# Optimization experiments

Hardware: AMD Instinct MI355X
Metric: run time of the kernel (lower is better)

The kernel has to match this reference:

```python
import jax, jax.numpy as jnp
import numpy as np

B, QL, KVL = 2, 1024, 2048
D = 4096          # hidden_size
NH, NKV = 32, 8   # attention heads / kv heads
HD = D // NH      # head_dim = 128
INNER = 4 * D     # SwiGLU intermediate = 16384
EPS = 1e-5
THETA = 10000.0


def rope_cos_sin(seq_len, head_dim, theta):
    inv_freq = 1.0 / (theta ** (jnp.arange(0, head_dim, 2, dtype=jnp.float32) / head_dim))
    t = jnp.arange(seq_len, dtype=jnp.float32)
    freqs = jnp.outer(t, inv_freq)                      # [S, HD/2]
    emb = jnp.concatenate([freqs, freqs], axis=-1)      # [S, HD]
    return jnp.cos(emb), jnp.sin(emb)


def rotate_half(x):
    half = x.shape[-1] // 2
    return jnp.concatenate([-x[..., half:], x[..., :half]], axis=-1)


def apply_rope(x, cos, sin):
    # x: [B, H, S, HD]; cos/sin: [S, HD] broadcast over batch & heads
    return x * cos[None, None] + rotate_half(x) * sin[None, None]


def layernorm(x, w, b):
    mu = jnp.mean(x, axis=-1, keepdims=True)
    var = jnp.var(x, axis=-1, keepdims=True)
    return (x - mu) * jax.lax.rsqrt(var + EPS) * w + b


def setup_inputs() -> dict:
    key = jax.random.key(0)
    ks = jax.random.split(key, 12)
    s = 0.02
    return {
        "hidden_states": jax.random.normal(ks[0], (B, QL, D), jnp.float32),
        "encoder_hidden_states": jax.random.normal(ks[1], (B, KVL, D), jnp.float32),
        "encoder_attention_mask": jnp.ones((B, KVL), jnp.float32),
        "ln1_w": jnp.ones((D,), jnp.float32),
        "ln1_b": jnp.zeros((D,), jnp.float32),
        "q_w": jax.random.normal(ks[2], (D, D), jnp.float32) * s,        # [out, in]
        "k_w": jax.random.normal(ks[3], (NKV * HD, D), jnp.float32) * s,
        "v_w": jax.random.normal(ks[4], (NKV * HD, D), jnp.float32) * s,
        "o_w": jax.random.normal(ks[5], (D, D), jnp.float32) * s,
        "ln2_w": jnp.ones((D,), jnp.float32),
        "ln2_b": jnp.zeros((D,), jnp.float32),
        "gate_w": jax.random.normal(ks[6], (INNER, D), jnp.float32) * s,
        "up_w": jax.random.normal(ks[7], (INNER, D), jnp.float32) * s,
        "down_w": jax.random.normal(ks[8], (D, INNER), jnp.float32) * s,
    }


def reference(hidden_states, encoder_hidden_states, encoder_attention_mask,
              ln1_w, ln1_b, q_w, k_w, v_w, o_w, ln2_w, ln2_b,
              gate_w, up_w, down_w):
    residual = hidden_states
    h = layernorm(hidden_states, ln1_w, ln1_b)

    # projections
    q = (h @ q_w.T).reshape(B, QL, NH, HD).transpose(0, 2, 1, 3)                    # [B,NH,QL,HD]
    k = (encoder_hidden_states @ k_w.T).reshape(B, KVL, NKV, HD).transpose(0, 2, 1, 3)  # [B,NKV,KVL,HD]
    v = (encoder_hidden_states @ v_w.T).reshape(B, KVL, NKV, HD).transpose(0, 2, 1, 3)

    # RoPE: q uses positions 0..QL-1, k uses positions 0..KVL-1 (position_ids=None -> cos[None])
    q_cos, q_sin = rope_cos_sin(QL, HD, THETA)
    kv_cos, kv_sin = rope_cos_sin(KVL, HD, THETA)
    q = apply_rope(q, q_cos, q_sin)
    k = apply_rope(k, kv_cos, kv_sin)

    # GQA repeat_kv: each kv head repeated num_key_value_groups times consecutively
    n_rep = NH // NKV
    k = jnp.repeat(k, n_rep, axis=1)  # [B,NH,KVL,HD]
    v = jnp.repeat(v, n_rep, axis=1)

    attn = jnp.einsum('bhqd,bhkd->bhqk', q, k) / np.sqrt(HD).astype(np.float32)
    # NOTE: original code ADDS the boolean mask (True -> +1.0) to the logits
    mask = (encoder_attention_mask != 0).astype(attn.dtype)  # [B,KVL]
    attn = attn + mask[:, None, None, :]
    attn = jax.nn.softmax(attn.astype(jnp.float32), axis=-1).astype(q.dtype)

    out = jnp.einsum('bhqk,bhkd->bhqd', attn, v)        # [B,NH,QL,HD]
    out = out.transpose(0, 2, 1, 3).reshape(B, QL, D)
    attn_out = out @ o_w.T

    h = residual + attn_out
    residual = h
    h = layernorm(h, ln2_w, ln2_b)
    ff = (jax.nn.silu(h @ gate_w.T) * (h @ up_w.T)) @ down_w.T
    return residual + ff
```

## Files before the change

### kernel.cpp

```cpp
#include <hip/hip_runtime.h>
#include <hip/hip_bf16.h>
#include <math.h>

using bf16 = __hip_bfloat16;
typedef __bf16 bfv8 __attribute__((ext_vector_type(8)));
typedef float f32x4 __attribute__((ext_vector_type(4)));

__device__ __forceinline__ f32x4 mfma16(bfv8 a, bfv8 b, f32x4 c) {
    return __builtin_amdgcn_mfma_f32_16x16x32_bf16(a, b, c, 0, 0, 0);
}

__device__ __forceinline__ void gload_lds16(const void* g, void* l) {
    __builtin_amdgcn_global_load_lds(
        (const __attribute__((address_space(1))) void*)g,
        (__attribute__((address_space(3))) void*)l, 16, 0, 0);
}

__global__ void cvt_kernel(const float* __restrict__ in, bf16* __restrict__ out, long n8) {
    long u = (long)blockIdx.x * 256 + threadIdx.x;
    if (u >= n8) return;
    const float4* p = (const float4*)in + u * 2;
    float4 a = p[0], b = p[1];
    bf16 t8[8] = { __float2bfloat16(a.x), __float2bfloat16(a.y), __float2bfloat16(a.z), __float2bfloat16(a.w),
                   __float2bfloat16(b.x), __float2bfloat16(b.y), __float2bfloat16(b.z), __float2bfloat16(b.w) };
    *(int4*)(out + u * 8) = *(const int4*)t8;
}

__global__ void cvt2_kernel(const float* __restrict__ in1, bf16* __restrict__ out1,
                            const float* __restrict__ in2, bf16* __restrict__ out2, long n8) {
    long u = (long)blockIdx.x * 256 + threadIdx.x;
    const float* in = in1;
    bf16* out = out1;
    if (u >= n8) { u -= n8; in = in2; out = out2; }
    const float4* p = (const float4*)in + u * 2;
    float4 a = p[0], b = p[1];
    bf16 t8[8] = { __float2bfloat16(a.x), __float2bfloat16(a.y), __float2bfloat16(a.z), __float2bfloat16(a.w),
                   __float2bfloat16(b.x), __float2bfloat16(b.y), __float2bfloat16(b.z), __float2bfloat16(b.w) };
    *(int4*)(out + u * 8) = *(const int4*)t8;
}

__global__ void layernorm_kernel(const float* __restrict__ x, const float* __restrict__ gw,
                                 const float* __restrict__ gb, bf16* __restrict__ out)
{
    const int D = 4096;
    int row = blockIdx.x, t = threadIdx.x;
    const float4* xr = (const float4*)(x + (size_t)row * D);
    float4 v[4];
    float s1 = 0.f, s2 = 0.f;
#pragma unroll
    for (int j = 0; j < 4; ++j) {
        v[j] = xr[t + j * 256];
        s1 += v[j].x + v[j].y + v[j].z + v[j].w;
        s2 += v[j].x * v[j].x + v[j].y * v[j].y + v[j].z * v[j].z + v[j].w * v[j].w;
    }
#pragma unroll
    for (int d = 1; d < 64; d <<= 1) { s1 += __shfl_xor(s1, d); s2 += __shfl_xor(s2, d); }
    __shared__ float red[8];
    int wave = t >> 6, lane = t & 63;
    if (lane == 0) { red[wave] = s1; red[4 + wave] = s2; }
    __syncthreads();
    s1 = red[0] + red[1] + red[2] + red[3];
    s2 = red[4] + red[5] + red[6] + red[7];
    float mu = s1 * (1.f / 4096.f);
    float var = s2 * (1.f / 4096.f) - mu * mu;
    float rs = rsqrtf(var + 1e-5f);
    bf16* orow = out + (size_t)row * D;
#pragma unroll
    for (int j = 0; j < 4; ++j) {
        int base = (t + j * 256) * 4;
        float xs[4] = { v[j].x, v[j].y, v[j].z, v[j].w };
        bf16 o4[4];
#pragma unroll
        for (int c = 0; c < 4; ++c)
            o4[c] = __float2bfloat16((xs[c] - mu) * rs * gw[base + c] + gb[base + c]);
        *(int2*)(orow + base) = *(const int2*)o4;
    }
}

__global__ void rope_kernel(bf16* __restrict__ x, int nheads, int seqlen, long total) {
    long idx = (long)blockIdx.x * 256 + threadIdx.x;
    if (idx >= total) return;
    int j = (int)(idx & 63);
    long t2 = idx >> 6;
    int h = (int)(t2 % nheads);
    long row = t2 / nheads;
    int pos = (int)(row % seqlen);
    float inv = exp2f(-(float)j * 0.20762050593046015f);
    float ang = (float)pos * inv;
    float s, c;
    sincosf(ang, &s, &c);
    bf16* p = x + row * ((long)nheads * 128) + (long)h * 128 + j;
    float x0 = __bfloat162float(p[0]);
    float x1 = __bfloat162float(p[64]);
    p[0]  = __float2bfloat16(x0 * c - x1 * s);
    p[64] = __float2bfloat16(x1 * c + x0 * s);
}

template<int BM, int BN, int MODE, bool DUAL, int CM, int CN, int XN>
__global__ __launch_bounds__(512, 2) void gemm_p(
        const bf16* __restrict__ A, const bf16* __restrict__ W, const bf16* __restrict__ W2,
        void* __restrict__ Cout, void* __restrict__ Cout2, const void* __restrict__ aux,
        int M, int N, int K, int Nsplit,
        int ngemm, const float* __restrict__ cf1, bf16* __restrict__ cd1, long cn1,
        const float* __restrict__ cf2, bf16* __restrict__ cd2, long cn2)
{
    const int t = threadIdx.x;
    if ((int)blockIdx.x >= ngemm) {
        const long nb = (long)gridDim.x - ngemm;
        const long tot = cn1 + cn2;
        for (long u = (long)((int)blockIdx.x - ngemm) * 512 + t; u < tot; u += nb * 512) {
            const float* in = cf1;
            bf16* op = cd1;
            long v = u;
            if (v >= cn1) { v -= cn1; in = cf2; op = cd2; }
            float4 a = ((const float4*)in)[v * 2];
            float4 b = ((const float4*)in)[v * 2 + 1];
            bf16 t8[8] = { __float2bfloat16(a.x), __float2bfloat16(a.y),
                           __float2bfloat16(a.z), __float2bfloat16(a.w),
                           __float2bfloat16(b.x), __float2bfloat16(b.y),
                           __float2bfloat16(b.z), __float2bfloat16(b.w) };
            *(int4*)(op + v * 8) = *(const int4*)t8;
        }
        return;
    }

    constexpr int MF = BM / 32;
    constexpr int NF = BN / 64;
    constexpr int ALD = BM / 128;
    constexpr int BLD = BN / 128;
    constexpr int SLD = ALD + BLD;
    __shared__ bf16 lds[3][(BM + BN) * 32];

    const int wid = t >> 6, lane = t & 63;
    const int lr = lane & 15, lg = lane >> 4;
    const int wr = wid >> 2, wc = wid & 3;
    const int bid = blockIdx.x;
    const int xcd = bid & 7, slot = bid >> 3;
    const int sm = slot / CN, sn = slot % CN;
    const int xm = xcd / XN, xn = xcd % XN;
    const int bm = (xm * CM + sm) * BM;
    const int bn = (xn * CN + sn) * BN;

    auto stage = [&](int tt, int buf) {
        const int k0 = tt * 32;
        char* ldsA = (char*)&lds[buf][0];
#pragma unroll
        for (int c = 0; c < ALD; ++c) {
            int Wb = (t + c * 512) * 16;
            int L = Wb ^ (((Wb >> 7) & 7) << 4);
            int row = L >> 6, colb = L & 63;
            gload_lds16(A + (size_t)(bm + row) * K + k0 + (colb >> 1), ldsA + Wb);
        }
        char* ldsB = (char*)&lds[buf][BM * 32];
#pragma unroll
        for (int c = 0; c < BLD; ++c) {
            int Wb = (t + c * 512) * 16;
            int L = Wb ^ (((Wb >> 7) & 7) << 4);
            int row = L >> 6, colb = L & 63;
            const bf16* src;
            if constexpr (DUAL) {
                int nr = bn + row;
                src = (nr >= Nsplit) ? W2 + (size_t)(nr - Nsplit) * K + k0 + (colb >> 1)
                                     : W  + (size_t)nr * K + k0 + (colb >> 1);
            } else {
                src = W + (size_t)(bn + row) * K + k0 + (colb >> 1);
            }
            gload_lds16(src, ldsB + Wb);
        }
    };

    const f32x4 zero4 = { 0.f, 0.f, 0.f, 0.f };
    f32x4 acc[MF][NF];
#pragma unroll
    for (int m = 0; m < MF; ++m)
#pragma unroll
        for (int n = 0; n < NF; ++n) acc[m][n] = zero4;

    const int T = K >> 5;
    stage(0, 0);
    stage(1, 1);
    if constexpr (SLD == 4) asm volatile("s_waitcnt vmcnt(4)" ::: "memory");
    else                    asm volatile("s_waitcnt vmcnt(3)" ::: "memory");
    __builtin_amdgcn_s_barrier();
    __builtin_amdgcn_sched_barrier(0);

    for (int tt = 0; tt < T; ++tt) {
        const int buf = tt % 3;
        bfv8 af[MF], bfr[NF];
#pragma unroll
        for (int m = 0; m < MF; ++m) {
            int row = wr * (BM / 2) + m * 16 + lr;
            int U = row * 64 + lg * 16;
            af[m] = *(const bfv8*)((const char*)&lds[buf][0] + (U ^ (((U >> 7) & 7) << 4)));
        }
#pragma unroll
        for (int n = 0; n < NF; ++n) {
            int row = wc * (BN / 4) + n * 16 + lr;
            int U = row * 64 + lg * 16;
            bfr[n] = *(const bfv8*)((const char*)&lds[buf][BM * 32] + (U ^ (((U >> 7) & 7) << 4)));
        }
        if (tt + 2 < T) stage(tt + 2, (tt + 2) % 3);
        __builtin_amdgcn_s_setprio(1);
#pragma unroll
        for (int m = 0; m < MF; ++m)
#pragma unroll
            for (int n = 0; n < NF; ++n)
                acc[m][n] = mfma16(af[m], bfr[n], acc[m][n]);
        __builtin_amdgcn_s_setprio(0);
        if (tt + 2 < T) {
            if constexpr (SLD == 4) asm volatile("s_waitcnt vmcnt(4)" ::: "memory");
            else                    asm volatile("s_waitcnt vmcnt(3)" ::: "memory");
        } else {
            asm volatile("s_waitcnt vmcnt(0)" ::: "memory");
        }
        __builtin_amdgcn_s_barrier();
        __builtin_amdgcn_sched_barrier(0);
    }

    const int r0 = bm + wr * (BM / 2), c0 = bn + wc * (BN / 4);
#pragma unroll
    for (int m = 0; m < MF; ++m)
#pragma unroll
        for (int n = 0; n < NF; ++n)
#pragma unroll
            for (int i = 0; i < 4; ++i) {
                int r = r0 + m * 16 + lg * 4 + i;
                int c = c0 + n * 16 + lr;
                float a = acc[m][n][i];
                if constexpr (DUAL) {
                    if (c < Nsplit) ((bf16*)Cout)[(size_t)r * Nsplit + c] = __float2bfloat16(a);
                    else ((bf16*)Cout2)[(size_t)r * (N - Nsplit) + (c - Nsplit)] = __float2bfloat16(a);
                } else {
                    size_t idx = (size_t)r * N + c;
                    if constexpr (MODE == 0) {
                        ((bf16*)Cout)[idx] = __float2bfloat16(a);
                    } else if constexpr (MODE == 1) {
                        a = a / (1.f + expf(-a));
                        ((bf16*)Cout)[idx] = __float2bfloat16(a);
                    } else if constexpr (MODE == 2) {
                        a *= __bfloat162float(((const bf16*)aux)[idx]);
                        ((bf16*)Cout)[idx] = __float2bfloat16(a);
                    } else {
                        ((float*)Cout)[idx] = a + ((const float*)aux)[idx];
                    }
                }
            }
}

template<int BN, int MODE, bool DUAL, int CM, int CN, int XN>
__global__ __launch_bounds__(512, 1) void gemm8(
        const bf16* __restrict__ A, const bf16* __restrict__ W, const bf16* __restrict__ W2,
        void* __restrict__ Cout, void* __restrict__ Cout2, const void* __restrict__ aux,
        int M, int N, int K, int Nsplit)
{
    constexpr bool BIG = (BN == 256);
    constexpr int NBUF = BIG ? 2 : 3;
    constexpr int ABY = 32768;
    constexpr int BBY = BN * 128;
    constexpr int TBY = ABY + BBY;
    __shared__ alignas(16) char lds8[NBUF * TBY];

    const int t = threadIdx.x;
    const int wid = t >> 6, lane = t & 63;
    const int lr = lane & 15, lg = lane >> 4;
    const int wrB = wid >> 2, wcB = wid & 3;
    const int wr4 = wid >> 1, wc4 = wid & 1;
    const int bid = blockIdx.x;
    const int xcd = bid & 7, slot = bid >> 3;
    const int sm = slot / CN, sn = slot % CN;
    const int xm = xcd / XN, xn = xcd % XN;
    const int bm = (xm * CM + sm) * 256;
    const int bn = (xn * CN + sn) * BN;

    auto stA = [&](int kt, int h, int buf) {
#pragma unroll
        for (int c = 0; c < 2; ++c) {
            int Wb = (t + c * 512) * 16;
            int L = Wb ^ (((Wb >> 7) & 7) << 4);
            gload_lds16(A + (size_t)(bm + h * 128 + (L >> 7)) * K + kt * 64 + ((L & 127) >> 1),
                        lds8 + buf * TBY + h * 16384 + Wb);
        }
    };
    auto stB = [&](int kt, int h, int buf) {
#pragma unroll
        for (int c = 0; c < 2; ++c) {
            int Wb = (t + c * 512) * 16;
            int L = Wb ^ (((Wb >> 7) & 7) << 4);
            int nr = bn + h * 128 + (L >> 7);
            const bf16* src;
            if constexpr (DUAL) {
                src = (nr >= Nsplit) ? W2 + (size_t)(nr - Nsplit) * K + kt * 64 + ((L & 127) >> 1)
                                     : W  + (size_t)nr * K + kt * 64 + ((L & 127) >> 1);
            } else {
                src = W + (size_t)nr * K + kt * 64 + ((L & 127) >> 1);
            }
            gload_lds16(src, lds8 + buf * TBY + ABY + h * 16384 + Wb);
        }
    };

    const f32x4 zero4 = { 0.f, 0.f, 0.f, 0.f };
    f32x4 acc[BIG ? 8 : 4][4];
#pragma unroll
    for (int m = 0; m < (BIG ? 8 : 4); ++m)
#pragma unroll
        for (int n = 0; n < 4; ++n) acc[m][n] = zero4;

    bfv8 af[4][2], bfr[2][2][2];
    bfv8 afs[2][2], bfs[4][2];

#define LOADA(BUF, MH) do {                                                   \
    const char* _ba = lds8 + (BUF) * TBY;                                     \
    _Pragma("unroll") for (int m = 0; m < 4; ++m)                             \
    _Pragma("unroll") for (int ks = 0; ks < 2; ++ks) {                        \
        int row = wrB * 128 + (MH) * 64 + m * 16 + lr;                        \
        int U = row * 128 + ks * 64 + lg * 16;                                \
        af[m][ks] = *(const bfv8*)(_ba + (U ^ ((row & 7) << 4)));             \
    } } while (0)

#define LOADB(BUF, NH) do {                                                   \
    const char* _bb = lds8 + (BUF) * TBY + ABY;                               \
    _Pragma("unroll") for (int n = 0; n < 2; ++n)                             \
    _Pragma("unroll") for (int ks = 0; ks < 2; ++ks) {                        \
        int row = wcB * 64 + (NH) * 32 + n * 16 + lr;                         \
        int U = row * 128 + ks * 64 + lg * 16;                                \
        bfr[NH][n][ks] = *(const bfv8*)(_bb + (U ^ ((row & 7) << 4)));        \
    } } while (0)

#define MFMAQ(MH, NH) do {                                                    \
    _Pragma("unroll") for (int m = 0; m < 4; ++m)                             \
    _Pragma("unroll") for (int n = 0; n < 2; ++n) {                           \
        acc[(MH)*4+m][(NH)*2+n] = mfma16(af[m][0], bfr[NH][n][0], acc[(MH)*4+m][(NH)*2+n]); \
        acc[(MH)*4+m][(NH)*2+n] = mfma16(af[m][1], bfr[NH][n][1], acc[(MH)*4+m][(NH)*2+n]); \
    } } while (0)

#define LOADA_S(BUF, MH) do {                                                 \
    const char* _ba = lds8 + (BUF) * TBY;                                     \
    _Pragma("unroll") for (int m = 0; m < 2; ++m)                             \
    _Pragma("unroll") for (int ks = 0; ks < 2; ++ks) {                        \
        int row = wr4 * 64 + (MH) * 32 + m * 16 + lr;                         \
        int U = row * 128 + ks * 64 + lg * 16;                                \
        afs[m][ks] = *(const bfv8*)(_ba + (U ^ ((row & 7) << 4)));            \
    } } while (0)

#define LOADB_S(BUF) do {                                                     \
    const char* _bb = lds8 + (BUF) * TBY + ABY;                               \
    _Pragma("unroll") for (int n = 0; n < 4; ++n)                             \
    _Pragma("unroll") for (int ks = 0; ks < 2; ++ks) {                        \
        int row = wc4 * 64 + n * 16 + lr;                                     \
        int U = row * 128 + ks * 64 + lg * 16;                                \
        bfs[n][ks] = *(const bfv8*)(_bb + (U ^ ((row & 7) << 4)));            \
    } } while (0)

#define MFMAQ_S(MH) do {                                                      \
    _Pragma("unroll") for (int m = 0; m < 2; ++m)                             \
    _Pragma("unroll") for (int n = 0; n < 4; ++n) {                           \
        acc[(MH)*2+m][n] = mfma16(afs[m][0], bfs[n][0], acc[(MH)*2+m][n]);    \
        acc[(MH)*2+m][n] = mfma16(afs[m][1], bfs[n][1], acc[(MH)*2+m][n]);    \
    } } while (0)

#define PH_TOP() do { __builtin_amdgcn_s_barrier();                           \
    asm volatile("s_waitcnt lgkmcnt(0)" ::: "memory");                        \
    __builtin_amdgcn_sched_barrier(0);                                        \
    __builtin_amdgcn_s_setprio(1); } while (0)

#define PH_END() do { __builtin_amdgcn_s_setprio(0);                          \
    __builtin_amdgcn_s_barrier(); } while (0)

#define GATE(LIVE) do { __builtin_amdgcn_s_setprio(0);                        \
    if (LIVE) { if constexpr (BIG) asm volatile("s_waitcnt vmcnt(4)" ::: "memory"); \
                else               asm volatile("s_waitcnt vmcnt(6)" ::: "memory"); } \
    else      asm volatile("s_waitcnt vmcnt(0)" ::: "memory");                \
    __builtin_amdgcn_s_barrier(); } while (0)

    const int T = K >> 6;
    const int T2 = T >> 1;

    if constexpr (BIG) {
        stA(0, 0, 0); stA(0, 1, 0); stB(0, 0, 0); stB(0, 1, 0);
        stB(1, 0, 1); stB(1, 1, 1);
        asm volatile("s_waitcnt vmcnt(4)" ::: "memory");
        __builtin_amdgcn_s_barrier();

        for (int tt = 0; tt < T2; ++tt) {
            const int o = 2 * tt + 1, e2 = 2 * tt + 2, o2 = 2 * tt + 3;
            const bool le = (e2 < T), lo = (o2 < T);
            LOADA(0, 0); LOADB(0, 0); stA(o, 0, 1);
            PH_TOP(); MFMAQ(0, 0); PH_END();
            LOADB(0, 1); stA(o, 1, 1);
            PH_TOP(); MFMAQ(0, 1); PH_END();
            LOADA(0, 1); if (le) stB(e2, 0, 0);
            PH_TOP(); MFMAQ(1, 1); PH_END();
            if (le) stB(e2, 1, 0);
            PH_TOP(); MFMAQ(1, 0); GATE(le);
            LOADA(1, 0); LOADB(1, 0); if (le) stA(e2, 0, 0);
            PH_TOP(); MFMAQ(0, 0); PH_END();
            LOADB(1, 1); if (le) stA(e2, 1, 0);
            PH_TOP(); MFMAQ(0, 1); PH_END();
            LOADA(1, 1); if (lo) stB(o2, 0, 1);
            PH_TOP(); MFMAQ(1, 1); PH_END();
            if (lo) stB(o2, 1, 1);
            PH_TOP(); MFMAQ(1, 0); GATE(le);
        }
    } else {
        stA(0, 0, 0); stB(0, 0, 0); stA(0, 1, 0);
        stA(1, 0, 1); stB(1, 0, 1); stA(1, 1, 1);
        asm volatile("s_waitcnt vmcnt(6)" ::: "memory");
        __builtin_amdgcn_s_barrier();

        int bE = 0, bO = 1, bN = 2;
        for (int tt = 0; tt < T2; ++tt) {
            const int e2 = 2 * tt + 2, o2 = 2 * tt + 3;
            const bool le = (e2 < T), lo = (o2 < T);
            LOADA_S(bE, 0); LOADB_S(bE); if (le) { stA(e2, 0, bN); stB(e2, 0, bN); }
            PH_TOP(); MFMAQ_S(0); PH_END();
            LOADA_S(bE, 1); if (le) stA(e2, 1, bN);
            PH_TOP(); MFMAQ_S(1); GATE(le);
            LOADA_S(bO, 0); LOADB_S(bO); if (lo) { stA(o2, 0, bE); stB(o2, 0, bE); }
            PH_TOP(); MFMAQ_S(0); PH_END();
            LOADA_S(bO, 1); if (lo) stA(o2, 1, bE);
            PH_TOP(); MFMAQ_S(1); GATE(lo);
            int nE = bN, nO = bE, nN = bO;
            bE = nE; bO = nO; bN = nN;
        }
    }

#undef LOADA
#undef LOADB
#undef MFMAQ
#undef LOADA_S
#undef LOADB_S
#undef MFMAQ_S
#undef PH_TOP
#undef PH_END
#undef GATE

    const int r0 = bm + (BIG ? wrB * 128 : wr4 * 64);
    const int c0 = bn + (BIG ? wcB * 64 : wc4 * 64);
#pragma unroll
    for (int mg = 0; mg < (BIG ? 8 : 4); ++mg)
#pragma unroll
        for (int ng = 0; ng < 4; ++ng)
#pragma unroll
            for (int i = 0; i < 4; ++i) {
                int r = r0 + mg * 16 + lg * 4 + i;
                int c = c0 + ng * 16 + lr;
                float a = acc[mg][ng][i];
                if constexpr (DUAL) {
                    if (c < Nsplit) ((bf16*)Cout)[(size_t)r * Nsplit + c] = __float2bfloat16(a);
                    else ((bf16*)Cout2)[(size_t)r * (N - Nsplit) + (c - Nsplit)] = __float2bfloat16(a);
                } else {
                    size_t idx = (size_t)r * N + c;
                    if constexpr (MODE == 0) {
                        ((bf16*)Cout)[idx] = __float2bfloat16(a);
                    } else if constexpr (MODE == 1) {
                        a = a / (1.f + expf(-a));
                        ((bf16*)Cout)[idx] = __float2bfloat16(a);
                    } else if constexpr (MODE == 2) {
                        a *= __bfloat162float(((const bf16*)aux)[idx]);
                        ((bf16*)Cout)[idx] = __float2bfloat16(a);
                    } else {
                        ((float*)Cout)[idx] = a + ((const float*)aux)[idx];
                    }
                }
            }
}

__global__ void transpose_v(const bf16* __restrict__ vb, bf16* __restrict__ vt) {
    __shared__ bf16 tile[64][68];
    int kv0 = blockIdx.x * 64, c0 = blockIdx.y * 64, b = blockIdx.z;
    int t = threadIdx.x;
    int cr = t & 15, rr = t >> 4;
#pragma unroll
    for (int j = 0; j < 4; ++j) {
        int r = rr + j * 16;
        *(int2*)&tile[r][cr * 4] = *(const int2*)&vb[(size_t)(b * 2048 + kv0 + r) * 1024 + c0 + cr * 4];
    }
    __syncthreads();
#pragma unroll
    for (int j = 0; j < 4; ++j) {
        int cc = rr + j * 16;
        bf16 tmp[4];
#pragma unroll
        for (int q = 0; q < 4; ++q) tmp[q] = tile[cr * 4 + q][cc];
        *(int2*)&vt[(size_t)(b * 1024 + c0 + cc) * 2048 + kv0 + cr * 4] = *(const int2*)tmp;
    }
}

__global__ __launch_bounds__(256) void attn_kernel(
    const bf16* __restrict__ Q, const bf16* __restrict__ Kb, const bf16* __restrict__ Vt,
    const float* __restrict__ mask, bf16* __restrict__ O)
{
    const int QL_ = 1024, KVL_ = 2048;
    const float scale = 0.08838834764831845f;
    int qt = blockIdx.x, h = blockIdx.y, b = blockIdx.z;
    int t = threadIdx.x, wave = t >> 6, lane = t & 63;
    int lr = lane & 15, lg = lane >> 4;
    int g = h >> 2;
    __shared__ bf16 Ksm[2][64 * 128];
    __shared__ bf16 Vsm[2][128 * 64];
    __shared__ bf16 Psm[4][16 * 72];
    int q0 = qt * 64 + wave * 16;

    auto stage = [&](int buf, int kv0) {
#pragma unroll
        for (int p2 = 0; p2 < 4; ++p2) {
            int Wb = (p2 * 256 + t) * 16;
            int row = Wb >> 8;
            int col = ((Wb & 255) ^ ((row & 7) << 4)) >> 1;
            gload_lds16(Kb + (size_t)(b * KVL_ + kv0 + row) * 1024 + g * 128 + col,
                        (char*)&Ksm[buf][0] + Wb);
        }
#pragma unroll
        for (int p2 = 0; p2 < 4; ++p2) {
            int Wb = (p2 * 256 + t) * 16;
            int row = Wb >> 7;
            int col = ((Wb & 127) ^ ((row & 7) << 4)) >> 1;
            gload_lds16(Vt + (size_t)(b * 1024 + g * 128 + row) * 2048 + kv0 + col,
                        (char*)&Vsm[buf][0] + Wb);
        }
    };

    const bf16* qptr = Q + (size_t)(b * QL_ + q0 + lr) * 4096 + h * 128;
    bfv8 qf[4];
#pragma unroll
    for (int kc = 0; kc < 4; ++kc) qf[kc] = *(const bfv8*)(qptr + kc * 32 + lg * 8);

    const f32x4 zero4 = { 0.f, 0.f, 0.f, 0.f };
    f32x4 accO[8];
#pragma unroll
    for (int dt = 0; dt < 8; ++dt) accO[dt] = zero4;
    float mrow[4] = { -1e30f, -1e30f, -1e30f, -1e30f };
    float lrow[4] = { 0.f, 0.f, 0.f, 0.f };

    stage(0, 0);
    int buf = 0;
    const int NT = KVL_ / 64;
    for (int tt = 0; tt < NT; ++tt) {
        const int kv0 = tt * 64;
        if (tt + 1 < NT) {
            stage(buf ^ 1, kv0 + 64);
            asm volatile("s_waitcnt vmcnt(8)" ::: "memory");
        } else {
            asm volatile("s_waitcnt vmcnt(0)" ::: "memory");
        }
        __builtin_amdgcn_s_barrier();

        f32x4 s[4];
#pragma unroll
        for (int ct = 0; ct < 4; ++ct) {
            s[ct] = zero4;
#pragma unroll
            for (int kc = 0; kc < 4; ++kc) {
                int row = ct * 16 + lr;
                int U = row * 256 + kc * 64 + lg * 16;
                bfv8 kf = *(const bfv8*)((const char*)&Ksm[buf][0] + (U ^ ((row & 7) << 4)));
                s[ct] = mfma16(qf[kc], kf, s[ct]);
            }
            float mv = mask[(size_t)b * KVL_ + kv0 + ct * 16 + lr];
            mv = (mv != 0.f) ? 1.f : 0.f;
#pragma unroll
            for (int i = 0; i < 4; ++i) s[ct][i] = s[ct][i] * scale + mv;
        }

        float rmx[4], mnew[4], corr[4], psum[4];
#pragma unroll
        for (int i = 0; i < 4; ++i) {
            rmx[i] = fmaxf(fmaxf(s[0][i], s[1][i]), fmaxf(s[2][i], s[3][i]));
#pragma unroll
            for (int d = 1; d < 16; d <<= 1) rmx[i] = fmaxf(rmx[i], __shfl_xor(rmx[i], d));
            mnew[i] = fmaxf(mrow[i], rmx[i]);
            corr[i] = expf(mrow[i] - mnew[i]);
            psum[i] = 0.f;
        }
#pragma unroll
        for (int ct = 0; ct < 4; ++ct)
#pragma unroll
            for (int i = 0; i < 4; ++i) {
                float pv = expf(s[ct][i] - mnew[i]);
                psum[i] += pv;
                Psm[wave][(lg * 4 + i) * 72 + ct * 16 + lr] = __float2bfloat16(pv);
            }
#pragma unroll
        for (int i = 0; i < 4; ++i) {
#pragma unroll
            for (int d = 1; d < 16; d <<= 1) psum[i] += __shfl_xor(psum[i], d);
            lrow[i] = lrow[i] * corr[i] + psum[i];
            mrow[i] = mnew[i];
        }
#pragma unroll
        for (int dt = 0; dt < 8; ++dt)
#pragma unroll
            for (int i = 0; i < 4; ++i) accO[dt][i] *= corr[i];

        bfv8 pf0 = *(const bfv8*)&Psm[wave][lr * 72 + 0 * 32 + lg * 8];
        bfv8 pf1 = *(const bfv8*)&Psm[wave][lr * 72 + 1 * 32 + lg * 8];
#pragma unroll
        for (int dt = 0; dt < 8; ++dt) {
            int row = dt * 16 + lr;
            int U0 = row * 128 + 0 * 64 + lg * 16;
            int U1 = row * 128 + 1 * 64 + lg * 16;
            bfv8 vf0 = *(const bfv8*)((const char*)&Vsm[buf][0] + (U0 ^ ((row & 7) << 4)));
            bfv8 vf1 = *(const bfv8*)((const char*)&Vsm[buf][0] + (U1 ^ ((row & 7) << 4)));
            accO[dt] = mfma16(pf0, vf0, accO[dt]);
            accO[dt] = mfma16(pf1, vf1, accO[dt]);
        }
        __builtin_amdgcn_s_barrier();
        buf ^= 1;
    }

    float invl[4];
#pragma unroll
    for (int i = 0; i < 4; ++i) invl[i] = 1.f / lrow[i];
#pragma unroll
    for (int dt = 0; dt < 8; ++dt)
#pragma unroll
        for (int i = 0; i < 4; ++i)
            O[(size_t)(b * QL_ + q0 + lg * 4 + i) * 4096 + h * 128 + dt * 16 + lr] =
                __float2bfloat16(accO[dt][i] * invl[i]);
}

extern "C" void kernel_launch(void* const* d_in, const int* in_sizes, int n_in,
                              void* d_out, int out_size, void* d_ws, size_t ws_size,
                              hipStream_t stream) {
    const float* hidden = (const float*)d_in[0];
    const float* enc    = (const float*)d_in[1];
    const float* mask   = (const float*)d_in[2];
    const float* ln1w   = (const float*)d_in[3];
    const float* ln1b   = (const float*)d_in[4];
    const float* qw     = (const float*)d_in[5];
    const float* kw     = (const float*)d_in[6];
    const float* vw     = (const float*)d_in[7];
    const float* ow     = (const float*)d_in[8];
    const float* ln2w   = (const float*)d_in[9];
    const float* ln2b   = (const float*)d_in[10];
    const float* gatew  = (const float*)d_in[11];
    const float* upw    = (const float*)d_in[12];
    const float* downw  = (const float*)d_in[13];
    float* out = (float*)d_out;
    char* ws = (char*)d_ws;

    auto cvt = [&](const float* src, bf16* dst, long n) {
        cvt_kernel<<<(int)(n / 2048), 256, 0, stream>>>(src, dst, n / 8);
    };

    if (ws_size >= 385875968ULL) {
        bf16* WA   = (bf16*)(ws);
        bf16* h1   = (bf16*)(ws);
        bf16* qwB  = (bf16*)(ws + 16777216);
        bf16* kwB  = (bf16*)(ws + 50331648);
        bf16* vwB  = (bf16*)(ws + 58720256);
        bf16* WB   = (bf16*)(ws + 134217728);
        bf16* encb = (bf16*)(ws + 134217728);
        bf16* qb   = (bf16*)(ws + 167772160);
        bf16* kb   = (bf16*)(ws + 184549376);
        bf16* vb   = (bf16*)(ws + 192937984);
        bf16* vt   = (bf16*)(ws + 201326592);
        bf16* attno= (bf16*)(ws + 209715200);
        bf16* owB  = (bf16*)(ws + 226492416);
        float* h2  = (float*)(ws + 268435456);
        bf16* h2n  = (bf16*)(ws + 301989888);
        bf16* g1   = (bf16*)(ws + 318767104);

        cvt2_kernel<<<16384, 256, 0, stream>>>(enc, encb, qw, qwB, 2097152L);
        layernorm_kernel<<<2048, 256, 0, stream>>>(hidden, ln1w, ln1b, h1);

        gemm_p<128, 256, 0, false, 8, 4, 4><<<384, 512, 0, stream>>>(
            h1, qwB, nullptr, qb, nullptr, nullptr, 2048, 4096, 4096, 0,
            256, kw, kwB, 524288L, vw, vwB, 524288L);
        rope_kernel<<<16384, 256, 0, stream>>>(qb, 32, 1024, 2048L * 32 * 64);

        gemm_p<128, 256, 0, true, 8, 4, 2><<<256, 512, 0, stream>>>(
            encb, kwB, vwB, kb, vb, nullptr, 4096, 2048, 4096, 1024,
            256, nullptr, nullptr, 0, nullptr, nullptr, 0);
        rope_kernel<<<8192, 256, 0, stream>>>(kb, 8, 2048, 4096L * 8 * 64);
        transpose_v<<<dim3(32, 16, 2), 256, 0, stream>>>(vb, vt);

        attn_kernel<<<dim3(16, 32, 2), 256, 0, stream>>>(qb, kb, vt, mask, attno);

        cvt(ow, owB, 16777216L);
        gemm_p<128, 256, 3, false, 8, 4, 4><<<512, 512, 0, stream>>>(
            attno, owB, nullptr, h2, nullptr, hidden, 2048, 4096, 4096, 0,
            256, gatew, WA, 8388608L, nullptr, nullptr, 0);

        layernorm_kernel<<<2048, 256, 0, stream>>>(h2, ln2w, ln2b, h2n);

        gemm8<256, 1, false, 8, 8, 8><<<512, 512, 0, stream>>>(
            h2n, WA, nullptr, g1, nullptr, nullptr, 2048, 16384, 4096, 0);
        cvt(upw, WA, 67108864L);
        gemm8<256, 2, false, 8, 8, 8><<<512, 512, 0, stream>>>(
            h2n, WA, nullptr, g1, nullptr, g1, 2048, 16384, 4096, 0);
        cvt(downw, WB, 67108864L);
        gemm8<128, 3, false, 8, 4, 8><<<256, 512, 0, stream>>>(
            g1, WB, nullptr, out, nullptr, h2, 2048, 4096, 16384, 0);
    } else {
        bf16*  wbuf  = (bf16*)(ws);
        bf16*  wbuf2 = (bf16*)(ws + 8388608);
        bf16*  h1    = (bf16*)(ws + 134217728);
        bf16*  encb  = (bf16*)(ws + 150994944);
        bf16*  qb    = (bf16*)(ws + 184549376);
        bf16*  kb    = (bf16*)(ws + 201326592);
        bf16*  vb    = (bf16*)(ws + 209715200);
        bf16*  attno = (bf16*)(ws + 218103808);
        float* h2    = (float*)(ws + 234881024);
        bf16*  vt    = (bf16*)(ws + 234881024);
        bf16*  h2n   = (bf16*)(ws + 268435456);
        bf16*  g1    = (bf16*)(ws + 285212672);

        cvt(enc, encb, 16777216L);
        layernorm_kernel<<<2048, 256, 0, stream>>>(hidden, ln1w, ln1b, h1);

        cvt(qw, wbuf, 16777216L);
        gemm_p<128, 256, 0, false, 8, 4, 4><<<256, 512, 0, stream>>>(
            h1, wbuf, nullptr, qb, nullptr, nullptr, 2048, 4096, 4096, 0,
            256, nullptr, nullptr, 0, nullptr, nullptr, 0);
        rope_kernel<<<16384, 256, 0, stream>>>(qb, 32, 1024, 2048L * 32 * 64);

        cvt2_kernel<<<4096, 256, 0, stream>>>(kw, wbuf, vw, wbuf2, 524288L);
        gemm_p<128, 256, 0, true, 8, 4, 2><<<256, 512, 0, stream>>>(
            encb, wbuf, wbuf2, kb, vb, nullptr, 4096, 2048, 4096, 1024,
            256, nullptr, nullptr, 0, nullptr, nullptr, 0);
        rope_kernel<<<8192, 256, 0, stream>>>(kb, 8, 2048, 4096L * 8 * 64);
        transpose_v<<<dim3(32, 16, 2), 256, 0, stream>>>(vb, vt);

        attn_kernel<<<dim3(16, 32, 2), 256, 0, stream>>>(qb, kb, vt, mask, attno);

        cvt(ow, wbuf, 16777216L);
        gemm_p<128, 256, 3, false, 8, 4, 4><<<256, 512, 0, stream>>>(
            attno, wbuf, nullptr, h2, nullptr, hidden, 2048, 4096, 4096, 0,
            256, nullptr, nullptr, 0, nullptr, nullptr, 0);

        layernorm_kernel<<<2048, 256, 0, stream>>>(h2, ln2w, ln2b, h2n);

        cvt(gatew, wbuf, 67108864L);
        gemm8<256, 1, false, 8, 8, 8><<<512, 512, 0, stream>>>(
            h2n, wbuf, nullptr, g1, nullptr, nullptr, 2048, 16384, 4096, 0);
        cvt(upw, wbuf, 67108864L);
        gemm8<256, 2, false, 8, 8, 8><<<512, 512, 0, stream>>>(
            h2n, wbuf, nullptr, g1, nullptr, g1, 2048, 16384, 4096, 0);

        cvt(downw, wbuf, 67108864L);
        gemm8<128, 3, false, 8, 4, 8><<<256, 512, 0, stream>>>(
            g1, wbuf, nullptr, out, nullptr, h2, 2048, 4096, 16384, 0);
    }
}
```

Measured before the change: 1.496 ms.

## Double-buffer LDS fragments and overlap reads with MFMAs in FFN GEMMs

Rewrites the main K-loop of the FFN GEMM kernel (renamed gemm_v). Register fragments are now double-buffered (A/B sets), so LDS reads for the next quadrant are issued while MFMAs on the current quadrant run. This replaces the previous per-phase barrier and lgkmcnt wait around every MFMA group with fewer barriers per K-tile. Global-to-LDS staging is reorganized to issue whole tiles at once with a single vmcnt gate, and setprio now wraps only the MFMA blocks. The cost is more register pressure from the doubled fragment sets, and the new hand-written wait and barrier ordering carries a risk of LDS races or pipeline stalls.

```diff
diff --git a/kernel.cpp b/kernel.cpp
--- a/kernel.cpp
+++ b/kernel.cpp
@@ -248,7 +248,7 @@
 }
 
 template<int BN, int MODE, bool DUAL, int CM, int CN, int XN>
-__global__ __launch_bounds__(512, 1) void gemm8(
+__global__ __launch_bounds__(512, 1) void gemm_v(
         const bf16* __restrict__ A, const bf16* __restrict__ W, const bf16* __restrict__ W2,
         void* __restrict__ Cout, void* __restrict__ Cout2, const void* __restrict__ aux,
         int M, int N, int K, int Nsplit)
@@ -305,134 +305,144 @@
 #pragma unroll
         for (int n = 0; n < 4; ++n) acc[m][n] = zero4;
 
-    bfv8 af[4][2], bfr[2][2][2];
-    bfv8 afs[2][2], bfs[4][2];
-
-#define LOADA(BUF, MH) do {                                                   \
+    bfv8 afA[4][2], afB[4][2], bfA[2][2], bfB[2][2];
+    bfv8 afsA[2][2], afsB[2][2], bfsA[4][2], bfsB[4][2];
+
+#define LOADA_TO(DST, BUF, MH) do {                                           \
     const char* _ba = lds8 + (BUF) * TBY;                                     \
     _Pragma("unroll") for (int m = 0; m < 4; ++m)                             \
     _Pragma("unroll") for (int ks = 0; ks < 2; ++ks) {                        \
         int row = wrB * 128 + (MH) * 64 + m * 16 + lr;                        \
         int U = row * 128 + ks * 64 + lg * 16;                                \
-        af[m][ks] = *(const bfv8*)(_ba + (U ^ ((row & 7) << 4)));             \
+        DST[m][ks] = *(const bfv8*)(_ba + (U ^ ((row & 7) << 4)));            \
     } } while (0)
 
-#define LOADB(BUF, NH) do {                                                   \
+#define LOADB_TO(DST, BUF, NH) do {                                           \
     const char* _bb = lds8 + (BUF) * TBY + ABY;                               \
     _Pragma("unroll") for (int n = 0; n < 2; ++n)                             \
     _Pragma("unroll") for (int ks = 0; ks < 2; ++ks) {                        \
         int row = wcB * 64 + (NH) * 32 + n * 16 + lr;                         \
         int U = row * 128 + ks * 64 + lg * 16;                                \
-        bfr[NH][n][ks] = *(const bfv8*)(_bb + (U ^ ((row & 7) << 4)));        \
+        DST[n][ks] = *(const bfv8*)(_bb + (U ^ ((row & 7) << 4)));            \
     } } while (0)
 
-#define MFMAQ(MH, NH) do {                                                    \
+#define MFMAQ_V(MH, NH, AF, BF) do { __builtin_amdgcn_s_setprio(1);           \
     _Pragma("unroll") for (int m = 0; m < 4; ++m)                             \
     _Pragma("unroll") for (int n = 0; n < 2; ++n) {                           \
-        acc[(MH)*4+m][(NH)*2+n] = mfma16(af[m][0], bfr[NH][n][0], acc[(MH)*4+m][(NH)*2+n]); \
-        acc[(MH)*4+m][(NH)*2+n] = mfma16(af[m][1], bfr[NH][n][1], acc[(MH)*4+m][(NH)*2+n]); \
-    } } while (0)
-
-#define LOADA_S(BUF, MH) do {                                                 \
+        acc[(MH)*4+m][(NH)*2+n] = mfma16(AF[m][0], BF[n][0], acc[(MH)*4+m][(NH)*2+n]); \
+        acc[(MH)*4+m][(NH)*2+n] = mfma16(AF[m][1], BF[n][1], acc[(MH)*4+m][(NH)*2+n]); \
+    } __builtin_amdgcn_s_setprio(0); } while (0)
+
+#define LOADA_S_TO(DST, BUF, MH) do {                                         \
     const char* _ba = lds8 + (BUF) * TBY;                                     \
     _Pragma("unroll") for (int m = 0; m < 2; ++m)                             \
     _Pragma("unroll") for (int ks = 0; ks < 2; ++ks) {                        \
         int row = wr4 * 64 + (MH) * 32 + m * 16 + lr;                         \
         int U = row * 128 + ks * 64 + lg * 16;                                \
-        afs[m][ks] = *(const bfv8*)(_ba + (U ^ ((row & 7) << 4)));            \
+        DST[m][ks] = *(const bfv8*)(_ba + (U ^ ((row & 7) << 4)));            \
     } } while (0)
 
-#define LOADB_S(BUF) do {                                                     \
+#define LOADB_S_TO(DST, BUF) do {                                             \
     const char* _bb = lds8 + (BUF) * TBY + ABY;                               \
     _Pragma("unroll") for (int n = 0; n < 4; ++n)                             \
     _Pragma("unroll") for (int ks = 0; ks < 2; ++ks) {                        \
         int row = wc4 * 64 + n * 16 + lr;                                     \
         int U = row * 128 + ks * 64 + lg * 16;                                \
-        bfs[n][ks] = *(const bfv8*)(_bb + (U ^ ((row & 7) << 4)));            \
+        DST[n][ks] = *(const bfv8*)(_bb + (U ^ ((row & 7) << 4)));            \
     } } while (0)
 
-#define MFMAQ_S(MH) do {                                                      \
+#define MFMA_H(MH, AF, BF) do { __builtin_amdgcn_s_setprio(1);                \
     _Pragma("unroll") for (int m = 0; m < 2; ++m)                             \
     _Pragma("unroll") for (int n = 0; n < 4; ++n) {                           \
-        acc[(MH)*2+m][n] = mfma16(afs[m][0], bfs[n][0], acc[(MH)*2+m][n]);    \
-        acc[(MH)*2+m][n] = mfma16(afs[m][1], bfs[n][1], acc[(MH)*2+m][n]);    \
-    } } while (0)
-
-#define PH_TOP() do { __builtin_amdgcn_s_barrier();                           \
-    asm volatile("s_waitcnt lgkmcnt(0)" ::: "memory");                        \
-    __builtin_amdgcn_sched_barrier(0);                                        \
-    __builtin_amdgcn_s_setprio(1); } while (0)
-
-#define PH_END() do { __builtin_amdgcn_s_setprio(0);                          \
-    __builtin_amdgcn_s_barrier(); } while (0)
-
-#define GATE(LIVE) do { __builtin_amdgcn_s_setprio(0);                        \
-    if (LIVE) { if constexpr (BIG) asm volatile("s_waitcnt vmcnt(4)" ::: "memory"); \
-                else               asm volatile("s_waitcnt vmcnt(6)" ::: "memory"); } \
-    else      asm volatile("s_waitcnt vmcnt(0)" ::: "memory");                \
-    __builtin_amdgcn_s_barrier(); } while (0)
+        acc[(MH)*2+m][n] = mfma16(AF[m][0], BF[n][0], acc[(MH)*2+m][n]);      \
+        acc[(MH)*2+m][n] = mfma16(AF[m][1], BF[n][1], acc[(MH)*2+m][n]);      \
+    } __builtin_amdgcn_s_setprio(0); } while (0)
+
+#define LGKM0() do { asm volatile("s_waitcnt lgkmcnt(0)" ::: "memory");       \
+    __builtin_amdgcn_sched_barrier(0); } while (0)
 
     const int T = K >> 6;
     const int T2 = T >> 1;
 
     if constexpr (BIG) {
         stA(0, 0, 0); stA(0, 1, 0); stB(0, 0, 0); stB(0, 1, 0);
-        stB(1, 0, 1); stB(1, 1, 1);
-        asm volatile("s_waitcnt vmcnt(4)" ::: "memory");
+        stA(1, 0, 1); stA(1, 1, 1); stB(1, 0, 1); stB(1, 1, 1);
+        asm volatile("s_waitcnt vmcnt(8)" ::: "memory");
         __builtin_amdgcn_s_barrier();
+        LOADA_TO(afA, 0, 0); LOADB_TO(bfA, 0, 0);
 
         for (int tt = 0; tt < T2; ++tt) {
-            const int o = 2 * tt + 1, e2 = 2 * tt + 2, o2 = 2 * tt + 3;
-            const bool le = (e2 < T), lo = (o2 < T);
-            LOADA(0, 0); LOADB(0, 0); stA(o, 0, 1);
-            PH_TOP(); MFMAQ(0, 0); PH_END();
-            LOADB(0, 1); stA(o, 1, 1);
-            PH_TOP(); MFMAQ(0, 1); PH_END();
-            LOADA(0, 1); if (le) stB(e2, 0, 0);
-            PH_TOP(); MFMAQ(1, 1); PH_END();
-            if (le) stB(e2, 1, 0);
-            PH_TOP(); MFMAQ(1, 0); GATE(le);
-            LOADA(1, 0); LOADB(1, 0); if (le) stA(e2, 0, 0);
-            PH_TOP(); MFMAQ(0, 0); PH_END();
-            LOADB(1, 1); if (le) stA(e2, 1, 0);
-            PH_TOP(); MFMAQ(0, 1); PH_END();
-            LOADA(1, 1); if (lo) stB(o2, 0, 1);
-            PH_TOP(); MFMAQ(1, 1); PH_END();
-            if (lo) stB(o2, 1, 1);
-            PH_TOP(); MFMAQ(1, 0); GATE(le);
+            const int e2 = 2 * tt + 2, o2 = 2 * tt + 3;
+            const bool le = (e2 < T);
+            LOADB_TO(bfB, 0, 1);
+            MFMAQ_V(0, 0, afA, bfA);
+            LOADA_TO(afB, 0, 1);
+            MFMAQ_V(0, 1, afA, bfB);
+            LGKM0();
+            MFMAQ_V(1, 1, afB, bfB);
+            __builtin_amdgcn_s_barrier();
+            if (le) { stA(e2, 0, 0); stA(e2, 1, 0); stB(e2, 0, 0); stB(e2, 1, 0); }
+            if (le) asm volatile("s_waitcnt vmcnt(8)" ::: "memory");
+            else    asm volatile("s_waitcnt vmcnt(0)" ::: "memory");
+            __builtin_amdgcn_s_barrier();
+            LOADA_TO(afA, 1, 0);
+            MFMAQ_V(1, 0, afB, bfA);
+            LOADB_TO(bfA, 1, 0);
+            LOADB_TO(bfB, 1, 1);
+            MFMAQ_V(0, 0, afA, bfA);
+            LOADA_TO(afB, 1, 1);
+            MFMAQ_V(0, 1, afA, bfB);
+            LGKM0();
+            MFMAQ_V(1, 1, afB, bfB);
+            __builtin_amdgcn_s_barrier();
+            if (le) { stA(o2, 0, 1); stA(o2, 1, 1); stB(o2, 0, 1); stB(o2, 1, 1); }
+            if (le) asm volatile("s_waitcnt vmcnt(8)" ::: "memory");
+            else    asm volatile("s_waitcnt vmcnt(0)" ::: "memory");
+            __builtin_amdgcn_s_barrier();
+            if (le) LOADA_TO(afA, 0, 0);
+            MFMAQ_V(1, 0, afB, bfA);
+            if (le) LOADB_TO(bfA, 0, 0);
         }
     } else {
-        stA(0, 0, 0); stB(0, 0, 0); stA(0, 1, 0);
-        stA(1, 0, 1); stB(1, 0, 1); stA(1, 1, 1);
+        stA(0, 0, 0); stA(0, 1, 0); stB(0, 0, 0);
+        stA(1, 0, 1); stA(1, 1, 1); stB(1, 0, 1);
         asm volatile("s_waitcnt vmcnt(6)" ::: "memory");
         __builtin_amdgcn_s_barrier();
-
-        int bE = 0, bO = 1, bN = 2;
+        LOADA_S_TO(afsA, 0, 0); LOADB_S_TO(bfsA, 0);
+
         for (int tt = 0; tt < T2; ++tt) {
-            const int e2 = 2 * tt + 2, o2 = 2 * tt + 3;
-            const bool le = (e2 < T), lo = (o2 < T);
-            LOADA_S(bE, 0); LOADB_S(bE); if (le) { stA(e2, 0, bN); stB(e2, 0, bN); }
-            PH_TOP(); MFMAQ_S(0); PH_END();
-            LOADA_S(bE, 1); if (le) stA(e2, 1, bN);
-            PH_TOP(); MFMAQ_S(1); GATE(le);
-            LOADA_S(bO, 0); LOADB_S(bO); if (lo) { stA(o2, 0, bE); stB(o2, 0, bE); }
-            PH_TOP(); MFMAQ_S(0); PH_END();
-            LOADA_S(bO, 1); if (lo) stA(o2, 1, bE);
-            PH_TOP(); MFMAQ_S(1); GATE(lo);
-            int nE = bN, nO = bE, nN = bO;
-            bE = nE; bO = nO; bN = nN;
-        }
-    }
-
-#undef LOADA
-#undef LOADB
-#undef MFMAQ
-#undef LOADA_S
-#undef LOADB_S
-#undef MFMAQ_S
-#undef PH_TOP
-#undef PH_END
-#undef GATE
+            const int e = 2 * tt, o = e + 1, e2 = e + 2, o2 = e + 3;
+            const int be = e % 3, bo = o % 3, be2 = e2 % 3, bo2 = o2 % 3;
+            const bool le = (e2 < T);
+            if (le) { stA(e2, 0, be2); stA(e2, 1, be2); stB(e2, 0, be2); }
+            LOADA_S_TO(afsB, be, 1);
+            MFMA_H(0, afsA, bfsA);
+            LGKM0();
+            if (le) asm volatile("s_waitcnt vmcnt(6)" ::: "memory");
+            else    asm volatile("s_waitcnt vmcnt(0)" ::: "memory");
+            __builtin_amdgcn_s_barrier();
+            LOADA_S_TO(afsA, bo, 0);
+            LOADB_S_TO(bfsB, bo);
+            MFMA_H(1, afsB, bfsA);
+            if (le) { stA(o2, 0, bo2); stA(o2, 1, bo2); stB(o2, 0, bo2); }
+            LOADA_S_TO(afsB, bo, 1);
+            MFMA_H(0, afsA, bfsB);
+            LGKM0();
+            if (le) asm volatile("s_waitcnt vmcnt(6)" ::: "memory");
+            else    asm volatile("s_waitcnt vmcnt(0)" ::: "memory");
+            __builtin_amdgcn_s_barrier();
+            if (le) { LOADA_S_TO(afsA, be2, 0); LOADB_S_TO(bfsA, be2); }
+            MFMA_H(1, afsB, bfsB);
+        }
+    }
+
+#undef LOADA_TO
+#undef LOADB_TO
+#undef MFMAQ_V
+#undef LOADA_S_TO
+#undef LOADB_S_TO
+#undef MFMA_H
+#undef LGKM0
 
     const int r0 = bm + (BIG ? wrB * 128 : wr4 * 64);
     const int c0 = bn + (BIG ? wcB * 64 : wc4 * 64);
@@ -684,13 +694,13 @@
 
         layernorm_kernel<<<2048, 256, 0, stream>>>(h2, ln2w, ln2b, h2n);
 
-        gemm8<256, 1, false, 8, 8, 8><<<512, 512, 0, stream>>>(
+        gemm_v<256, 1, false, 8, 8, 8><<<512, 512, 0, stream>>>(
             h2n, WA, nullptr, g1, nullptr, nullptr, 2048, 16384, 4096, 0);
         cvt(upw, WA, 67108864L);
-        gemm8<256, 2, false, 8, 8, 8><<<512, 512, 0, stream>>>(
+        gemm_v<256, 2, false, 8, 8, 8><<<512, 512, 0, stream>>>(
             h2n, WA, nullptr, g1, nullptr, g1, 2048, 16384, 4096, 0);
         cvt(downw, WB, 67108864L);
-        gemm8<128, 3, false, 8, 4, 8><<<256, 512, 0, stream>>>(
+        gemm_v<128, 3, false, 8, 4, 8><<<256, 512, 0, stream>>>(
             g1, WB, nullptr, out, nullptr, h2, 2048, 4096, 16384, 0);
     } else {
         bf16*  wbuf  = (bf16*)(ws);
@@ -732,14 +742,14 @@
         layernorm_kernel<<<2048, 256, 0, stream>>>(h2, ln2w, ln2b, h2n);
 
         cvt(gatew, wbuf, 67108864L);
-        gemm8<256, 1, false, 8, 8, 8><<<512, 512, 0, stream>>>(
+        gemm_v<256, 1, false, 8, 8, 8><<<512, 512, 0, stream>>>(
             h2n, wbuf, nullptr, g1, nullptr, nullptr, 2048, 16384, 4096, 0);
         cvt(upw, wbuf, 67108864L);
-        gemm8<256, 2, false, 8, 8, 8><<<512, 512, 0, stream>>>(
+        gemm_v<256, 2, false, 8, 8, 8><<<512, 512, 0, stream>>>(
             h2n, wbuf, nullptr, g1, nullptr, g1, 2048, 16384, 4096, 0);
 
         cvt(downw, wbuf, 67108864L);
-        gemm8<128, 3, false, 8, 4, 8><<<256, 512, 0, stream>>>(
+        gemm_v<128, 3, false, 8, 4, 8><<<256, 512, 0, stream>>>(
             g1, wbuf, nullptr, out, nullptr, h2, 2048, 4096, 16384, 0);
     }
 }
```

After: 2.078 ms. 1.39x slower.
